# Kernel optimization log

Hardware: AMD Instinct MI355X
Metric: run time of the kernel (lower is better)

Reference implementation:

```python
import jax, jax.numpy as jnp
import numpy as np

N_NODES = 50000
N_EDGES = 800000
D_IN, D_HID, D_OUT = 128, 128, 64


def setup_inputs() -> dict:
    key = jax.random.key(0)
    ks = jax.random.split(key, 8)
    x = jax.random.normal(ks[0], (N_NODES, D_IN), dtype=jnp.float32)
    edge_index = jax.random.randint(ks[1], (2, N_EDGES), 0, N_NODES, dtype=jnp.int64)
    s1 = 1.0 / np.sqrt(D_IN)
    s2 = 1.0 / np.sqrt(D_HID)
    # PyG SAGEConv: out = lin_l(mean_aggr(x_j)) + lin_r(x_root); bias lives in lin_l
    Wl1 = jax.random.uniform(ks[2], (D_HID, D_IN), jnp.float32, -s1, s1)
    bl1 = jnp.zeros((D_HID,), jnp.float32)
    Wr1 = jax.random.uniform(ks[3], (D_HID, D_IN), jnp.float32, -s1, s1)
    Wl2 = jax.random.uniform(ks[4], (D_OUT, D_HID), jnp.float32, -s2, s2)
    bl2 = jnp.zeros((D_OUT,), jnp.float32)
    Wr2 = jax.random.uniform(ks[5], (D_OUT, D_HID), jnp.float32, -s2, s2)
    return {"x": x, "edge_index": edge_index, "Wl1": Wl1, "bl1": bl1, "Wr1": Wr1,
            "Wl2": Wl2, "bl2": bl2, "Wr2": Wr2}


def _sage_conv(x, src, dst, Wl, bl, Wr):
    # mean aggregation of source-node features onto destination nodes
    msg = x[src]                                              # [E, d]
    agg = jax.ops.segment_sum(msg, dst, num_segments=N_NODES)  # [N, d]
    cnt = jax.ops.segment_sum(jnp.ones((src.shape[0],), x.dtype), dst,
                              num_segments=N_NODES)            # [N]
    mean = agg / jnp.maximum(cnt, 1.0)[:, None]
    return mean @ Wl.T + bl + x @ Wr.T


def reference(x, edge_index, Wl1, bl1, Wr1, Wl2, bl2, Wr2):
    src, dst = edge_index[0], edge_index[1]
    h = jax.nn.relu(_sage_conv(x, src, dst, Wl1, bl1, Wr1))
    h = jax.nn.relu(_sage_conv(h, src, dst, Wl2, bl2, Wr2))
    return jax.nn.log_softmax(h, axis=-1)
```

## Files before the change

### kernel.cpp

```cpp
#include <hip/hip_runtime.h>
#include <cstdint>
#include <cstddef>

#define N_NODES 50000
#define N_EDGES 800000
#define ROWS_PAD 50048
#define ZROW 50000
#define BUCKET_CAP 64

typedef _Float16 f16;
typedef _Float16 f16x2 __attribute__((ext_vector_type(2)));
typedef _Float16 f16x8 __attribute__((ext_vector_type(8)));
typedef float f32x4 __attribute__((ext_vector_type(4)));
typedef unsigned short us4 __attribute__((ext_vector_type(4)));


#define EPT 16
#define CHUNK (256 * EPT)
#define NCHUNK ((N_EDGES + CHUNK - 1) / CHUNK)
#define NB_FILL (NCHUNK * 8)
#define NB_CX 3125
#define NB_CW 192
#define RANGE_SZ (N_NODES / 8)

__global__ __launch_bounds__(256) void preprocess_kernel(
    const int* __restrict__ edge, int* __restrict__ cnt, unsigned short* __restrict__ bucket,
    const float* __restrict__ x, f16* __restrict__ X16, f16* __restrict__ H16,
    const float* __restrict__ Wl1, const float* __restrict__ Wr1,
    const float* __restrict__ Wl2, const float* __restrict__ Wr2,
    f16* __restrict__ Wc1, f16* __restrict__ Wc2) {
  const int b = blockIdx.x;
  const int tid = threadIdx.x;
  if (b < NB_FILL) {
    const int r = b & 7, chunk = b >> 3;
    const int lo = r * RANGE_SZ, hi = lo + RANGE_SZ;
    const int base = chunk * CHUNK + tid;
    #pragma unroll
    for (int i = 0; i < EPT; ++i) {
      const int e = base + i * 256;
      if (e < N_EDGES) {
        const int dst = edge[N_EDGES + e];
        if (dst >= lo && dst < hi) {
          const int src = edge[e];
          const int pos = atomicAdd(&cnt[dst], 1);
          if (pos < BUCKET_CAP) bucket[(size_t)dst * BUCKET_CAP + pos] = (unsigned short)src;
        }
      }
    }
  } else if (b < NB_FILL + NB_CX) {
    const int idx = (b - NB_FILL) * 256 + tid;
    const int row = idx >> 4, c8 = idx & 15;
    const float4 v0 = *reinterpret_cast<const float4*>(x + (size_t)row * 128 + c8 * 8);
    const float4 v1 = *reinterpret_cast<const float4*>(x + (size_t)row * 128 + c8 * 8 + 4);
    f16x8 o;
    o[0] = (f16)v0.x; o[1] = (f16)v0.y; o[2] = (f16)v0.z; o[3] = (f16)v0.w;
    o[4] = (f16)v1.x; o[5] = (f16)v1.y; o[6] = (f16)v1.z; o[7] = (f16)v1.w;
    *reinterpret_cast<f16x8*>(X16 + (size_t)row * 128 + c8 * 8) = o;
  } else if (b < NB_FILL + NB_CX + NB_CW) {
    const int idx = (b - NB_FILL - NB_CX) * 256 + tid;
    if (idx < 128 * 256) {
      const int n = idx >> 8, k = idx & 255;
      Wc1[idx] = (f16)((k < 128) ? Wl1[n * 128 + k] : Wr1[n * 128 + (k - 128)]);
    } else {
      const int j = idx - 128 * 256;
      const int n = j >> 8, k = j & 255;
      Wc2[j] = (f16)((k < 128) ? Wl2[n * 128 + k] : Wr2[n * 128 + (k - 128)]);
    }
  } else {
    if (tid < 64)
      reinterpret_cast<f16x2*>(X16 + (size_t)ZROW * 128)[tid] = (f16x2){(f16)0.f, (f16)0.f};
    else if (tid < 128)
      reinterpret_cast<f16x2*>(H16 + (size_t)ZROW * 128)[tid - 64] = (f16x2){(f16)0.f, (f16)0.f};
  }
}


__device__ __forceinline__ void aggregate_to_lds(
    const f16* __restrict__ F, const int* __restrict__ cnt,
    const unsigned short* __restrict__ bucket,
    f16 (*M)[136], int wid, int lane) {
  const int quad = lane >> 4, l16 = lane & 15;
  #pragma unroll 1
  for (int g = 0; g < 4; ++g) {
    const int nb = blockIdx.x * 64 + wid * 16 + g * 4;
    const int node = nb + quad;
    const int dv = (lane < 4) ? cnt[nb + lane] : 0;
    const int dq = __shfl(dv, quad, 64);
    const int dqc = min(dq, BUCKET_CAP);
    int md = max(max(__shfl(dv, 0, 64), __shfl(dv, 1, 64)),
                 max(__shfl(dv, 2, 64), __shfl(dv, 3, 64)));
    md = min(md, BUCKET_CAP);
    const us4 b4 = *reinterpret_cast<const us4*>(bucket + (size_t)node * BUCKET_CAP + l16 * 4);
    float acc[8];
    #pragma unroll
    for (int c = 0; c < 8; ++c) acc[c] = 0.f;
    const f16* Fsrc = F + l16 * 8;
    for (int j = 0; j < md; j += 16) {
      f16x8 v[16];
      #pragma unroll
      for (int k = 0; k < 16; ++k) {
        const int slot = j + k;
        const int idx = __shfl((int)b4[k & 3], quad * 16 + (slot >> 2), 64);
        const int row = (slot < dqc) ? idx : ZROW;
        v[k] = *reinterpret_cast<const f16x8*>(Fsrc + (size_t)row * 128);
      }
      #pragma unroll
      for (int k = 0; k < 16; ++k) {
        #pragma unroll
        for (int c = 0; c < 8; ++c) acc[c] += (float)v[k][c];
      }
    }
    const float inv = 1.0f / (float)(dq > 0 ? dq : 1);
    f16x8 o;
    #pragma unroll
    for (int c = 0; c < 8; ++c) o[c] = (f16)(acc[c] * inv);
    *reinterpret_cast<f16x8*>(&M[wid * 16 + g * 4 + quad][l16 * 8]) = o;
  }
}


__global__ __launch_bounds__(256, 4) void layer1_kernel(
    const f16* __restrict__ X16, const int* __restrict__ cnt,
    const unsigned short* __restrict__ bucket, const f16* __restrict__ Wc,
    const float* __restrict__ bias, f16* __restrict__ H16) {
  __shared__ f16 M[64][136];
  const int wid = threadIdx.x >> 6, lane = threadIdx.x & 63;
  const int quad = lane >> 4, l16 = lane & 15;
  aggregate_to_lds(X16, cnt, bucket, M, wid, lane);
  __syncthreads();
  const int row0 = blockIdx.x * 64 + wid * 16;
  f32x4 acc[8];
  #pragma unroll
  for (int u = 0; u < 8; ++u) acc[u] = (f32x4){0.f, 0.f, 0.f, 0.f};
  const f16x8* Wb = reinterpret_cast<const f16x8*>(Wc) + quad;
  const f16* Xrow = X16 + (size_t)(row0 + l16) * 128 + quad * 8;
  #pragma unroll
  for (int s = 0; s < 8; ++s) {
    const f16x8 a = (s < 4)
        ? *reinterpret_cast<const f16x8*>(&M[wid * 16 + l16][quad * 8 + s * 32])
        : *reinterpret_cast<const f16x8*>(Xrow + (s - 4) * 32);
    #pragma unroll
    for (int u = 0; u < 8; ++u) {
      const f16x8 bb = Wb[(u * 16 + l16) * 32 + s * 4];
      acc[u] = __builtin_amdgcn_mfma_f32_16x16x32_f16(a, bb, acc[u], 0, 0, 0);
    }
  }
  #pragma unroll
  for (int u = 0; u < 8; ++u) {
    const int col = u * 16 + l16;
    const float bv = bias[col];
    #pragma unroll
    for (int r = 0; r < 4; ++r) {
      const int row = row0 + quad * 4 + r;
      if (row < N_NODES)
        H16[(size_t)row * 128 + col] = (f16)fmaxf(acc[u][r] + bv, 0.f);
    }
  }
}


__global__ __launch_bounds__(256, 4) void layer2_kernel(
    const f16* __restrict__ H16, const int* __restrict__ cnt,
    const unsigned short* __restrict__ bucket, const f16* __restrict__ Wc,
    const float* __restrict__ bias, float* __restrict__ out) {
  __shared__ f16 M[64][136];
  const int wid = threadIdx.x >> 6, lane = threadIdx.x & 63;
  const int quad = lane >> 4, l16 = lane & 15;
  aggregate_to_lds(H16, cnt, bucket, M, wid, lane);
  __syncthreads();
  const int row0 = blockIdx.x * 64 + wid * 16;
  f32x4 acc[4];
  #pragma unroll
  for (int u = 0; u < 4; ++u) acc[u] = (f32x4){0.f, 0.f, 0.f, 0.f};
  const f16x8* Wb = reinterpret_cast<const f16x8*>(Wc) + quad;
  const f16* Hrow = H16 + (size_t)(row0 + l16) * 128 + quad * 8;
  #pragma unroll
  for (int s = 0; s < 8; ++s) {
    const f16x8 a = (s < 4)
        ? *reinterpret_cast<const f16x8*>(&M[wid * 16 + l16][quad * 8 + s * 32])
        : *reinterpret_cast<const f16x8*>(Hrow + (s - 4) * 32);
    #pragma unroll
    for (int u = 0; u < 4; ++u) {
      const f16x8 bb = Wb[(u * 16 + l16) * 32 + s * 4];
      acc[u] = __builtin_amdgcn_mfma_f32_16x16x32_f16(a, bb, acc[u], 0, 0, 0);
    }
  }
  float bv[4];
  #pragma unroll
  for (int u = 0; u < 4; ++u) bv[u] = bias[u * 16 + l16];
  #pragma unroll
  for (int r = 0; r < 4; ++r) {
    float v[4];
    #pragma unroll
    for (int u = 0; u < 4; ++u) v[u] = fmaxf(acc[u][r] + bv[u], 0.f);
    float m = fmaxf(fmaxf(v[0], v[1]), fmaxf(v[2], v[3]));
    #pragma unroll
    for (int off = 1; off < 16; off <<= 1) m = fmaxf(m, __shfl_xor(m, off, 64));
    float s = __expf(v[0] - m) + __expf(v[1] - m) + __expf(v[2] - m) + __expf(v[3] - m);
    #pragma unroll
    for (int off = 1; off < 16; off <<= 1) s += __shfl_xor(s, off, 64);
    const float ls = m + __logf(s);
    const int row = row0 + quad * 4 + r;
    if (row < N_NODES) {
      #pragma unroll
      for (int u = 0; u < 4; ++u)
        out[(size_t)row * 64 + u * 16 + l16] = v[u] - ls;
    }
  }
}


extern "C" void kernel_launch(void* const* d_in, const int* in_sizes, int n_in,
                              void* d_out, int out_size, void* d_ws, size_t ws_size,
                              hipStream_t stream) {
  const float* x   = (const float*)d_in[0];
  const int* edge  = (const int*)d_in[1];
  const float* Wl1 = (const float*)d_in[2];
  const float* bl1 = (const float*)d_in[3];
  const float* Wr1 = (const float*)d_in[4];
  const float* Wl2 = (const float*)d_in[5];
  const float* bl2 = (const float*)d_in[6];
  const float* Wr2 = (const float*)d_in[7];
  float* out = (float*)d_out;

  char* ws = (char*)d_ws;
  size_t off = 0;
  auto alloc = [&](size_t bytes) -> char* {
    char* p = ws + off;
    off = (off + bytes + 255) & ~(size_t)255;
    return p;
  };
  int* cnt               = (int*)alloc((size_t)ROWS_PAD * 4);
  unsigned short* bucket = (unsigned short*)alloc((size_t)ROWS_PAD * BUCKET_CAP * 2);
  f16* X16 = (f16*)alloc((size_t)ROWS_PAD * 128 * 2);
  f16* H16 = (f16*)alloc((size_t)ROWS_PAD * 128 * 2);
  f16* Wc1 = (f16*)alloc((size_t)128 * 256 * 2);
  f16* Wc2 = (f16*)alloc((size_t)64 * 256 * 2);

  hipMemsetAsync(cnt, 0, (size_t)ROWS_PAD * 4, stream);

  preprocess_kernel<<<NB_FILL + NB_CX + NB_CW + 1, 256, 0, stream>>>(
      edge, cnt, bucket, x, X16, H16, Wl1, Wr1, Wl2, Wr2, Wc1, Wc2);

  layer1_kernel<<<ROWS_PAD / 64, 256, 0, stream>>>(X16, cnt, bucket, Wc1, bl1, H16);
  layer2_kernel<<<ROWS_PAD / 64, 256, 0, stream>>>(H16, cnt, bucket, Wc2, bl2, out);
}
```

Baseline: 228.2 us.

## Halve rows per block, split GEMM columns across waves, use 16 dst ranges

The layer kernels now process 32 nodes per block instead of 64, which doubles the grid. The four waves split the dense GEMM as two row halves by two column halves. In layer 2 the log-softmax row max and sum are combined across the two column-half waves through shared memory and an extra barrier. Separately, the bucket-fill pass partitions destinations into 16 ranges instead of 8, which lowers atomic contention per block but reads the edge array twice as often. The aim is more parallelism and less serial gather per wave, at the cost of extra launches, barrier overhead and redundant edge reads.

```diff
diff --git a/kernel.cpp b/kernel.cpp
--- a/kernel.cpp
+++ b/kernel.cpp
@@ -15,13 +15,14 @@
 typedef unsigned short us4 __attribute__((ext_vector_type(4)));
 
 
+#define NRANGE 16
 #define EPT 16
 #define CHUNK (256 * EPT)
 #define NCHUNK ((N_EDGES + CHUNK - 1) / CHUNK)
-#define NB_FILL (NCHUNK * 8)
+#define NB_FILL (NCHUNK * NRANGE)
 #define NB_CX 3125
 #define NB_CW 192
-#define RANGE_SZ (N_NODES / 8)
+#define RANGE_SZ (N_NODES / NRANGE)
 
 __global__ __launch_bounds__(256) void preprocess_kernel(
     const int* __restrict__ edge, int* __restrict__ cnt, unsigned short* __restrict__ bucket,
@@ -32,7 +33,7 @@
   const int b = blockIdx.x;
   const int tid = threadIdx.x;
   if (b < NB_FILL) {
-    const int r = b & 7, chunk = b >> 3;
+    const int r = b & (NRANGE - 1), chunk = b >> 4;
     const int lo = r * RANGE_SZ, hi = lo + RANGE_SZ;
     const int base = chunk * CHUNK + tid;
     #pragma unroll
@@ -81,8 +82,8 @@
     f16 (*M)[136], int wid, int lane) {
   const int quad = lane >> 4, l16 = lane & 15;
   #pragma unroll 1
-  for (int g = 0; g < 4; ++g) {
-    const int nb = blockIdx.x * 64 + wid * 16 + g * 4;
+  for (int g = 0; g < 2; ++g) {
+    const int nb = blockIdx.x * 32 + wid * 8 + g * 4;
     const int node = nb + quad;
     const int dv = (lane < 4) ? cnt[nb + lane] : 0;
     const int dq = __shfl(dv, quad, 64);
@@ -114,7 +115,7 @@
     f16x8 o;
     #pragma unroll
     for (int c = 0; c < 8; ++c) o[c] = (f16)(acc[c] * inv);
-    *reinterpret_cast<f16x8*>(&M[wid * 16 + g * 4 + quad][l16 * 8]) = o;
+    *reinterpret_cast<f16x8*>(&M[wid * 8 + g * 4 + quad][l16 * 8]) = o;
   }
 }
 
@@ -123,37 +124,39 @@
     const f16* __restrict__ X16, const int* __restrict__ cnt,
     const unsigned short* __restrict__ bucket, const f16* __restrict__ Wc,
     const float* __restrict__ bias, f16* __restrict__ H16) {
-  __shared__ f16 M[64][136];
+  __shared__ f16 M[32][136];
   const int wid = threadIdx.x >> 6, lane = threadIdx.x & 63;
   const int quad = lane >> 4, l16 = lane & 15;
   aggregate_to_lds(X16, cnt, bucket, M, wid, lane);
   __syncthreads();
-  const int row0 = blockIdx.x * 64 + wid * 16;
-  f32x4 acc[8];
-  #pragma unroll
-  for (int u = 0; u < 8; ++u) acc[u] = (f32x4){0.f, 0.f, 0.f, 0.f};
+  const int rhalf = wid & 1, nhalf = wid >> 1;
+  const int row0 = blockIdx.x * 32 + rhalf * 16;
+  f32x4 acc[4];
+  #pragma unroll
+  for (int t = 0; t < 4; ++t) acc[t] = (f32x4){0.f, 0.f, 0.f, 0.f};
   const f16x8* Wb = reinterpret_cast<const f16x8*>(Wc) + quad;
   const f16* Xrow = X16 + (size_t)(row0 + l16) * 128 + quad * 8;
   #pragma unroll
   for (int s = 0; s < 8; ++s) {
     const f16x8 a = (s < 4)
-        ? *reinterpret_cast<const f16x8*>(&M[wid * 16 + l16][quad * 8 + s * 32])
+        ? *reinterpret_cast<const f16x8*>(&M[rhalf * 16 + l16][quad * 8 + s * 32])
         : *reinterpret_cast<const f16x8*>(Xrow + (s - 4) * 32);
     #pragma unroll
-    for (int u = 0; u < 8; ++u) {
+    for (int t = 0; t < 4; ++t) {
+      const int u = nhalf * 4 + t;
       const f16x8 bb = Wb[(u * 16 + l16) * 32 + s * 4];
-      acc[u] = __builtin_amdgcn_mfma_f32_16x16x32_f16(a, bb, acc[u], 0, 0, 0);
-    }
-  }
-  #pragma unroll
-  for (int u = 0; u < 8; ++u) {
-    const int col = u * 16 + l16;
+      acc[t] = __builtin_amdgcn_mfma_f32_16x16x32_f16(a, bb, acc[t], 0, 0, 0);
+    }
+  }
+  #pragma unroll
+  for (int t = 0; t < 4; ++t) {
+    const int col = (nhalf * 4 + t) * 16 + l16;
     const float bv = bias[col];
     #pragma unroll
     for (int r = 0; r < 4; ++r) {
       const int row = row0 + quad * 4 + r;
       if (row < N_NODES)
-        H16[(size_t)row * 128 + col] = (f16)fmaxf(acc[u][r] + bv, 0.f);
+        H16[(size_t)row * 128 + col] = (f16)fmaxf(acc[t][r] + bv, 0.f);
     }
   }
 }
@@ -163,48 +166,68 @@
     const f16* __restrict__ H16, const int* __restrict__ cnt,
     const unsigned short* __restrict__ bucket, const f16* __restrict__ Wc,
     const float* __restrict__ bias, float* __restrict__ out) {
-  __shared__ f16 M[64][136];
+  __shared__ f16 M[32][136];
+  __shared__ float PM[4][16], PS[4][16];
   const int wid = threadIdx.x >> 6, lane = threadIdx.x & 63;
   const int quad = lane >> 4, l16 = lane & 15;
   aggregate_to_lds(H16, cnt, bucket, M, wid, lane);
   __syncthreads();
-  const int row0 = blockIdx.x * 64 + wid * 16;
-  f32x4 acc[4];
-  #pragma unroll
-  for (int u = 0; u < 4; ++u) acc[u] = (f32x4){0.f, 0.f, 0.f, 0.f};
+  const int rhalf = wid & 1, nhalf = wid >> 1;
+  const int row0 = blockIdx.x * 32 + rhalf * 16;
+  f32x4 acc[2];
+  #pragma unroll
+  for (int t = 0; t < 2; ++t) acc[t] = (f32x4){0.f, 0.f, 0.f, 0.f};
   const f16x8* Wb = reinterpret_cast<const f16x8*>(Wc) + quad;
   const f16* Hrow = H16 + (size_t)(row0 + l16) * 128 + quad * 8;
   #pragma unroll
   for (int s = 0; s < 8; ++s) {
     const f16x8 a = (s < 4)
-        ? *reinterpret_cast<const f16x8*>(&M[wid * 16 + l16][quad * 8 + s * 32])
+        ? *reinterpret_cast<const f16x8*>(&M[rhalf * 16 + l16][quad * 8 + s * 32])
         : *reinterpret_cast<const f16x8*>(Hrow + (s - 4) * 32);
     #pragma unroll
-    for (int u = 0; u < 4; ++u) {
+    for (int t = 0; t < 2; ++t) {
+      const int u = nhalf * 2 + t;
       const f16x8 bb = Wb[(u * 16 + l16) * 32 + s * 4];
-      acc[u] = __builtin_amdgcn_mfma_f32_16x16x32_f16(a, bb, acc[u], 0, 0, 0);
-    }
-  }
-  float bv[4];
-  #pragma unroll
-  for (int u = 0; u < 4; ++u) bv[u] = bias[u * 16 + l16];
+      acc[t] = __builtin_amdgcn_mfma_f32_16x16x32_f16(a, bb, acc[t], 0, 0, 0);
+    }
+  }
+  float bv[2];
+  #pragma unroll
+  for (int t = 0; t < 2; ++t) bv[t] = bias[(nhalf * 2 + t) * 16 + l16];
+  float v[4][2], pm[4], ps[4];
   #pragma unroll
   for (int r = 0; r < 4; ++r) {
-    float v[4];
-    #pragma unroll
-    for (int u = 0; u < 4; ++u) v[u] = fmaxf(acc[u][r] + bv[u], 0.f);
-    float m = fmaxf(fmaxf(v[0], v[1]), fmaxf(v[2], v[3]));
+    #pragma unroll
+    for (int t = 0; t < 2; ++t) v[r][t] = fmaxf(acc[t][r] + bv[t], 0.f);
+    float m = fmaxf(v[r][0], v[r][1]);
     #pragma unroll
     for (int off = 1; off < 16; off <<= 1) m = fmaxf(m, __shfl_xor(m, off, 64));
-    float s = __expf(v[0] - m) + __expf(v[1] - m) + __expf(v[2] - m) + __expf(v[3] - m);
+    float s = __expf(v[r][0] - m) + __expf(v[r][1] - m);
     #pragma unroll
     for (int off = 1; off < 16; off <<= 1) s += __shfl_xor(s, off, 64);
-    const float ls = m + __logf(s);
+    pm[r] = m;
+    ps[r] = s;
+  }
+  if (l16 == 0) {
+    #pragma unroll
+    for (int r = 0; r < 4; ++r) {
+      PM[wid][quad * 4 + r] = pm[r];
+      PS[wid][quad * 4 + r] = ps[r];
+    }
+  }
+  __syncthreads();
+  #pragma unroll
+  for (int r = 0; r < 4; ++r) {
+    const float m2 = PM[wid ^ 2][quad * 4 + r];
+    const float s2 = PS[wid ^ 2][quad * 4 + r];
+    const float mt = fmaxf(pm[r], m2);
+    const float st = ps[r] * __expf(pm[r] - mt) + s2 * __expf(m2 - mt);
+    const float ls = mt + __logf(st);
     const int row = row0 + quad * 4 + r;
     if (row < N_NODES) {
       #pragma unroll
-      for (int u = 0; u < 4; ++u)
-        out[(size_t)row * 64 + u * 16 + l16] = v[u] - ls;
+      for (int t = 0; t < 2; ++t)
+        out[(size_t)row * 64 + (nhalf * 2 + t) * 16 + l16] = v[r][t] - ls;
     }
   }
 }
@@ -242,6 +265,6 @@
   preprocess_kernel<<<NB_FILL + NB_CX + NB_CW + 1, 256, 0, stream>>>(
       edge, cnt, bucket, x, X16, H16, Wl1, Wr1, Wl2, Wr2, Wc1, Wc2);
 
-  layer1_kernel<<<ROWS_PAD / 64, 256, 0, stream>>>(X16, cnt, bucket, Wc1, bl1, H16);
-  layer2_kernel<<<ROWS_PAD / 64, 256, 0, stream>>>(H16, cnt, bucket, Wc2, bl2, out);
-}
+  layer1_kernel<<<ROWS_PAD / 32, 256, 0, stream>>>(X16, cnt, bucket, Wc1, bl1, H16);
+  layer2_kernel<<<ROWS_PAD / 32, 256, 0, stream>>>(H16, cnt, bucket, Wc2, bl2, out);
+}
```

Result: no change. 227.7 us (-0.2%).
